# Optimization experiments

Hardware: AMD Instinct MI355X
Metric: run time of the kernel (lower is better)

## Reference

```python
import jax, jax.numpy as jnp
import numpy as np

OUTPUT_DIMS = (7, 7)  # adaptive target (H_out, W_out)
H_AXIS, W_AXIS = 1, 2  # NHWC ordering


def _adaptive_pool_axis(x, out_dim, axis):
    """Adaptive average pool along one axis.

    Matches the TF fallback: output i averages x[floor(i*in/out) : ceil((i+1)*in/out)].
    Implemented with a single cumulative sum + two gathers (windows vary in size).
    """
    in_dim = x.shape[axis]
    # Static (trace-time) window boundaries, identical to the TF floor/ceil math.
    idx = np.arange(out_dim, dtype=np.float64)
    starts = np.floor(idx * in_dim / out_dim).astype(np.int32)
    ends = np.ceil((idx + 1) * in_dim / out_dim).astype(np.int32)
    # Prefix sums with a leading zero so sum over [s, e) = cs[e] - cs[s].
    cs = jnp.cumsum(x, axis=axis)
    zero = jnp.zeros_like(jnp.take(cs, jnp.array([0]), axis=axis))
    cs = jnp.concatenate([zero, cs], axis=axis)  # length in_dim + 1 along axis
    sums = jnp.take(cs, jnp.asarray(ends), axis=axis) - jnp.take(cs, jnp.asarray(starts), axis=axis)
    counts = (ends - starts).astype(x.dtype)
    bshape = [1] * x.ndim
    bshape[axis] = out_dim
    return sums / counts.reshape(bshape)


def setup_inputs() -> dict:
    key = jax.random.key(0)
    inputs = jax.random.normal(key, (32, 50, 50, 768), dtype=jnp.float32)
    return {"inputs": inputs}


def reference(inputs):
    # Separable adaptive average pooling: H axis first, then W axis,
    # exactly as TFAdaptiveAvgPool2D.call does in the non-divisible case.
    h_pooled = _adaptive_pool_axis(inputs, OUTPUT_DIMS[0], H_AXIS)
    out = _adaptive_pool_axis(h_pooled, OUTPUT_DIMS[1], W_AXIS)
    return out
```

## Files before the change

kernel.cpp:

```cpp
#include <hip/hip_runtime.h>


#define N_  32
#define HIN 50
#define WIN 50
#define C_  768
#define HOUT 7
#define WOUT 7
#define CG (C_ / 4)
#define TOTAL (N_ * HOUT * WOUT * CG)

__global__ __launch_bounds__(256) void adaptive_pool_kernel(
    const float4* __restrict__ in, float4* __restrict__ out) {
    int idx = blockIdx.x * blockDim.x + threadIdx.x;
    if (idx >= TOTAL) return;

    int cg = idx % CG;
    int t  = idx / CG;
    int wo = t % WOUT; t /= WOUT;
    int ho = t % HOUT;
    int n  = t / HOUT;

    int hs = (ho * HIN) / HOUT;
    int ws = (wo * WIN) / WOUT;

    const float4* base = in + ((size_t)((n * HIN + hs) * WIN + ws)) * CG + cg;

    float4 acc = make_float4(0.f, 0.f, 0.f, 0.f);
    for (int dh = 0; dh < 8; ++dh) {
        const float4* rp = base + (size_t)dh * (WIN * CG);
        #pragma unroll
        for (int dw = 0; dw < 8; ++dw) {
            float4 v = rp[(size_t)dw * CG];
            acc.x += v.x; acc.y += v.y; acc.z += v.z; acc.w += v.w;
        }
    }
    const float s = 1.0f / 64.0f;
    acc.x *= s; acc.y *= s; acc.z *= s; acc.w *= s;
    out[idx] = acc;
}

extern "C" void kernel_launch(void* const* d_in, const int* in_sizes, int n_in,
                              void* d_out, int out_size, void* d_ws, size_t ws_size,
                              hipStream_t stream) {
    const float4* in  = (const float4*)d_in[0];
    float4*       out = (float4*)d_out;
    int threads = 256;
    int blocks = (TOTAL + threads - 1) / threads;
    adaptive_pool_kernel<<<blocks, threads, 0, stream>>>(in, out);
}
```

Before: 329.3 us.

## Split adaptive pooling into separable W-pass and H-pass kernels via workspace

Replaces the single kernel, where each thread summed an 8x8 window with 64 loads, with two kernels. The first pools along W into a workspace buffer, and the second pools that intermediate along H and applies the 1/64 scale. This gives many more threads, each with only 8 independent loads, which should expose more memory-level parallelism and avoid re-reading overlapping window rows. In exchange it writes and re-reads an intermediate buffer and adds a second kernel launch. Both kernels hardcode window start = 7*i with size 8, which is correct for 50->7.

Result: no change. 335.4 us (+1.8%).

```diff
diff --git a/kernel.cpp b/kernel.cpp
--- a/kernel.cpp
+++ b/kernel.cpp
@@ -1,19 +1,54 @@
 #include <hip/hip_runtime.h>
 
 
-#define N_  32
-#define HIN 50
-#define WIN 50
-#define C_  768
+#define N_   32
+#define HIN  50
+#define WIN  50
+#define C_   768
 #define HOUT 7
 #define WOUT 7
-#define CG (C_ / 4)
-#define TOTAL (N_ * HOUT * WOUT * CG)
+#define CG   (C_ / 4)
 
-__global__ __launch_bounds__(256) void adaptive_pool_kernel(
-    const float4* __restrict__ in, float4* __restrict__ out) {
+#define P1_TOTAL (N_ * HIN * WOUT * CG)
+#define P2_TOTAL (N_ * HOUT * WOUT * CG)
+
+__global__ __launch_bounds__(256) void pool_w_kernel(
+    const float4* __restrict__ in, float4* __restrict__ ws_out) {
     int idx = blockIdx.x * blockDim.x + threadIdx.x;
-    if (idx >= TOTAL) return;
+    if (idx >= P1_TOTAL) return;
+
+    int cg = idx % CG;
+    int t  = idx / CG;
+    int wo = t % WOUT; t /= WOUT;
+    int h  = t % HIN;
+    int n  = t / HIN;
+
+    int w0 = wo * 7;
+
+    const float4* base = in + ((size_t)((n * HIN + h) * WIN + w0)) * CG + cg;
+
+    float4 v0 = base[0 * CG];
+    float4 v1 = base[1 * CG];
+    float4 v2 = base[2 * CG];
+    float4 v3 = base[3 * CG];
+    float4 v4 = base[4 * CG];
+    float4 v5 = base[5 * CG];
+    float4 v6 = base[6 * CG];
+    float4 v7 = base[7 * CG];
+
+    float4 acc;
+    acc.x = (v0.x + v1.x) + (v2.x + v3.x) + ((v4.x + v5.x) + (v6.x + v7.x));
+    acc.y = (v0.y + v1.y) + (v2.y + v3.y) + ((v4.y + v5.y) + (v6.y + v7.y));
+    acc.z = (v0.z + v1.z) + (v2.z + v3.z) + ((v4.z + v5.z) + (v6.z + v7.z));
+    acc.w = (v0.w + v1.w) + (v2.w + v3.w) + ((v4.w + v5.w) + (v6.w + v7.w));
+
+    ws_out[idx] = acc;
+}
+
+__global__ __launch_bounds__(256) void pool_h_kernel(
+    const float4* __restrict__ ws_in, float4* __restrict__ out) {
+    int idx = blockIdx.x * blockDim.x + threadIdx.x;
+    if (idx >= P2_TOTAL) return;
 
     int cg = idx % CG;
     int t  = idx / CG;
@@ -21,22 +56,27 @@
     int ho = t % HOUT;
     int n  = t / HOUT;
 
-    int hs = (ho * HIN) / HOUT;
-    int ws = (wo * WIN) / WOUT;
+    int h0 = ho * 7;
 
-    const float4* base = in + ((size_t)((n * HIN + hs) * WIN + ws)) * CG + cg;
+    const float4* base = ws_in + ((size_t)((n * HIN + h0) * WOUT + wo)) * CG + cg;
+    const int rs = WOUT * CG;
 
-    float4 acc = make_float4(0.f, 0.f, 0.f, 0.f);
-    for (int dh = 0; dh < 8; ++dh) {
-        const float4* rp = base + (size_t)dh * (WIN * CG);
-        #pragma unroll
-        for (int dw = 0; dw < 8; ++dw) {
-            float4 v = rp[(size_t)dw * CG];
-            acc.x += v.x; acc.y += v.y; acc.z += v.z; acc.w += v.w;
-        }
-    }
+    float4 v0 = base[0 * rs];
+    float4 v1 = base[1 * rs];
+    float4 v2 = base[2 * rs];
+    float4 v3 = base[3 * rs];
+    float4 v4 = base[4 * rs];
+    float4 v5 = base[5 * rs];
+    float4 v6 = base[6 * rs];
+    float4 v7 = base[7 * rs];
+
     const float s = 1.0f / 64.0f;
-    acc.x *= s; acc.y *= s; acc.z *= s; acc.w *= s;
+    float4 acc;
+    acc.x = s * ((v0.x + v1.x) + (v2.x + v3.x) + ((v4.x + v5.x) + (v6.x + v7.x)));
+    acc.y = s * ((v0.y + v1.y) + (v2.y + v3.y) + ((v4.y + v5.y) + (v6.y + v7.y)));
+    acc.z = s * ((v0.z + v1.z) + (v2.z + v3.z) + ((v4.z + v5.z) + (v6.z + v7.z)));
+    acc.w = s * ((v0.w + v1.w) + (v2.w + v3.w) + ((v4.w + v5.w) + (v6.w + v7.w)));
+
     out[idx] = acc;
 }
 
@@ -45,7 +85,8 @@
                               hipStream_t stream) {
     const float4* in  = (const float4*)d_in[0];
     float4*       out = (float4*)d_out;
-    int threads = 256;
-    int blocks = (TOTAL + threads - 1) / threads;
-    adaptive_pool_kernel<<<blocks, threads, 0, stream>>>(in, out);
+    float4*       ws  = (float4*)d_ws;
+
+    pool_w_kernel<<<(P1_TOTAL + 255) / 256, 256, 0, stream>>>(in, ws);
+    pool_h_kernel<<<(P2_TOTAL + 255) / 256, 256, 0, stream>>>(ws, out);
 }
```

## Restructure pooling: one block per output row, threads split H window, LDS reduce

Applied to the files above, without the earlier changes.

Each block now handles one (n, ho) output row with 384 threads: two halves each sum 4 input rows over all 7 output columns for one channel group. The halves are combined through shared memory and written out. This replaces one thread per output element and is meant to cut index arithmetic and improve load coalescing and reuse. The cost is fewer, larger blocks (224) with more registers per thread, which may limit memory-level parallelism on a large GPU.

Measured after the change: 329.5 us. No clear change (+0.0%).

```diff
diff --git a/kernel.cpp b/kernel.cpp
--- a/kernel.cpp
+++ b/kernel.cpp
@@ -1,43 +1,74 @@
 #include <hip/hip_runtime.h>
 
 
-#define N_  32
-#define HIN 50
-#define WIN 50
-#define C_  768
+#define N_   32
+#define HIN  50
+#define WIN  50
+#define C_   768
 #define HOUT 7
 #define WOUT 7
-#define CG (C_ / 4)
-#define TOTAL (N_ * HOUT * WOUT * CG)
+#define CG   (C_ / 4)
 
-__global__ __launch_bounds__(256) void adaptive_pool_kernel(
+__global__ __launch_bounds__(384) void adaptive_pool_fused(
     const float4* __restrict__ in, float4* __restrict__ out) {
-    int idx = blockIdx.x * blockDim.x + threadIdx.x;
-    if (idx >= TOTAL) return;
+    __shared__ float4 lds[WOUT][CG];
 
-    int cg = idx % CG;
-    int t  = idx / CG;
-    int wo = t % WOUT; t /= WOUT;
-    int ho = t % HOUT;
-    int n  = t / HOUT;
+    const int bid = blockIdx.x;
+    const int n  = bid / HOUT;
+    const int ho = bid % HOUT;
+    const int h0 = ho * 7;
 
-    int hs = (ho * HIN) / HOUT;
-    int ws = (wo * WIN) / WOUT;
+    const int tid = threadIdx.x;
+    const int rh  = tid / CG;
+    const int cg  = tid % CG;
 
-    const float4* base = in + ((size_t)((n * HIN + hs) * WIN + ws)) * CG + cg;
+    float4 acc[WOUT];
+    #pragma unroll
+    for (int wo = 0; wo < WOUT; ++wo)
+        acc[wo] = make_float4(0.f, 0.f, 0.f, 0.f);
 
-    float4 acc = make_float4(0.f, 0.f, 0.f, 0.f);
-    for (int dh = 0; dh < 8; ++dh) {
-        const float4* rp = base + (size_t)dh * (WIN * CG);
+    const int hbase = h0 + rh * 4;
+    #pragma unroll
+    for (int dh = 0; dh < 4; ++dh) {
+        const float4* rp = in + ((size_t)((n * HIN + (hbase + dh)) * WIN)) * CG + cg;
         #pragma unroll
-        for (int dw = 0; dw < 8; ++dw) {
-            float4 v = rp[(size_t)dw * CG];
-            acc.x += v.x; acc.y += v.y; acc.z += v.z; acc.w += v.w;
+        for (int wo = 0; wo < WOUT; ++wo) {
+            const float4* wp = rp + (size_t)(wo * 7) * CG;
+            float4 v0 = wp[0 * CG];
+            float4 v1 = wp[1 * CG];
+            float4 v2 = wp[2 * CG];
+            float4 v3 = wp[3 * CG];
+            float4 v4 = wp[4 * CG];
+            float4 v5 = wp[5 * CG];
+            float4 v6 = wp[6 * CG];
+            float4 v7 = wp[7 * CG];
+            acc[wo].x += ((v0.x + v1.x) + (v2.x + v3.x)) + ((v4.x + v5.x) + (v6.x + v7.x));
+            acc[wo].y += ((v0.y + v1.y) + (v2.y + v3.y)) + ((v4.y + v5.y) + (v6.y + v7.y));
+            acc[wo].z += ((v0.z + v1.z) + (v2.z + v3.z)) + ((v4.z + v5.z) + (v6.z + v7.z));
+            acc[wo].w += ((v0.w + v1.w) + (v2.w + v3.w)) + ((v4.w + v5.w) + (v6.w + v7.w));
         }
     }
-    const float s = 1.0f / 64.0f;
-    acc.x *= s; acc.y *= s; acc.z *= s; acc.w *= s;
-    out[idx] = acc;
+
+    if (rh == 1) {
+        #pragma unroll
+        for (int wo = 0; wo < WOUT; ++wo)
+            lds[wo][cg] = acc[wo];
+    }
+    __syncthreads();
+
+    if (rh == 0) {
+        const float s = 1.0f / 64.0f;
+        float4* op = out + ((size_t)((n * HOUT + ho) * WOUT)) * CG + cg;
+        #pragma unroll
+        for (int wo = 0; wo < WOUT; ++wo) {
+            float4 o = lds[wo][cg];
+            o.x = s * (o.x + acc[wo].x);
+            o.y = s * (o.y + acc[wo].y);
+            o.z = s * (o.z + acc[wo].z);
+            o.w = s * (o.w + acc[wo].w);
+            op[(size_t)wo * CG] = o;
+        }
+    }
 }
 
 extern "C" void kernel_launch(void* const* d_in, const int* in_sizes, int n_in,
@@ -45,7 +76,5 @@
                               hipStream_t stream) {
     const float4* in  = (const float4*)d_in[0];
     float4*       out = (float4*)d_out;
-    int threads = 256;
-    int blocks = (TOTAL + threads - 1) / threads;
-    adaptive_pool_kernel<<<blocks, threads, 0, stream>>>(in, out);
+    adaptive_pool_fused<<<N_ * HOUT, 384, 0, stream>>>(in, out);
 }
```
